# Kernel tuning notes

Hardware: AMD Instinct MI355X
Metric: run time of the kernel (lower is better)

The kernel has to match this reference:

```python
import jax, jax.numpy as jnp
import numpy as np

B, S, D_IN, H, NH, L = 8, 1024, 512, 1024, 16, 4
HD = H // NH
SCALE = HD ** -0.5
EPS = 1e-5


def _ln(x, g, b):
    m = jnp.mean(x, axis=-1, keepdims=True)
    v = jnp.mean((x - m) ** 2, axis=-1, keepdims=True)
    return (x - m) * jax.lax.rsqrt(v + EPS) * g + b


def setup_inputs() -> dict:
    key = jax.random.key(0)
    ks = jax.random.split(key, 12)
    s = lambda k, shape, fan: jax.random.normal(k, shape, jnp.float32) * (fan ** -0.5)
    return {
        "x": jax.random.normal(ks[0], (B, S, D_IN), jnp.float32),
        "W_in": s(ks[1], (D_IN, H), D_IN), "b_in": jnp.zeros((H,), jnp.float32),
        "W_qkv": s(ks[2], (L, H, 3 * H), H), "b_qkv": jnp.zeros((L, 3 * H), jnp.float32),
        "W_o": s(ks[3], (L, H, H), H), "b_o": jnp.zeros((L, H), jnp.float32),
        "g1": jnp.ones((L, H), jnp.float32), "be1": jnp.zeros((L, H), jnp.float32),
        "W_out": s(ks[4], (H, H), H), "b_out": jnp.zeros((H,), jnp.float32),
        "g2": jnp.ones((H,), jnp.float32), "be2": jnp.zeros((H,), jnp.float32),
    }


def _attn_layer(x, Wqkv, bqkv, Wo, bo, g, be):
    b, s, h = x.shape
    qkv = (x @ Wqkv + bqkv).reshape(b, s, 3, NH, HD)
    q = qkv[:, :, 0].transpose(0, 2, 1, 3)  # [B,NH,S,HD]
    k = qkv[:, :, 1].transpose(0, 2, 1, 3)
    v = qkv[:, :, 2].transpose(0, 2, 1, 3)
    scores = jnp.einsum("bhqd,bhkd->bhqk", q, k) * SCALE
    w = jax.nn.softmax(scores, axis=-1)  # dropout is identity in eval
    o = jnp.einsum("bhqk,bhkd->bhqd", w, v)
    o = o.transpose(0, 2, 1, 3).reshape(b, s, h)
    return _ln(o @ Wo + bo + x, g, be)


def reference(x, W_in, b_in, W_qkv, b_qkv, W_o, b_o, g1, be1, W_out, b_out, g2, be2):
    h = x @ W_in + b_in
    for i in range(L):
        h = _attn_layer(h, W_qkv[i], b_qkv[i], W_o[i], b_o[i], g1[i], be1[i])
    pooled = jnp.mean(h, axis=1)  # [B,H]
    return _ln(pooled @ W_out + b_out, g2, be2)
```

## Files before the change

### kernel.cpp

```cpp
#include <hip/hip_runtime.h>
#include <stdint.h>

typedef unsigned short u16;
typedef unsigned int   u32;
typedef __attribute__((ext_vector_type(8))) short short8;
typedef __attribute__((ext_vector_type(4))) float f32x4;
typedef __attribute__((ext_vector_type(16))) float f32x16;
typedef __attribute__((ext_vector_type(2))) unsigned int uint2v;

#define B_   8
#define S_   1024
#define DIN_ 512
#define H_   1024
#define NH_  16
#define HD_  64
#define L_   4
#define M_   (B_*S_)
#define SCALE_ 0.125f
#define EPS_ 1e-5f

__device__ __forceinline__ u16 f2b(float f) {
  u32 u = __builtin_bit_cast(u32, f);
  u32 r = (u + 0x7fffu + ((u >> 16) & 1u)) >> 16;
  return (u16)r;
}

__device__ __forceinline__ u32 cvtpk(float lo, float hi) {
  u32 r;
  asm("v_cvt_pk_bf16_f32 %0, %1, %2" : "=v"(r) : "v"(lo), "v"(hi));
  return r;
}

__device__ __forceinline__ void gll16(const void* g, void* l) {
  __builtin_amdgcn_global_load_lds(
      (const __attribute__((address_space(1))) u32*)(uintptr_t)g,
      (__attribute__((address_space(3))) u32*)(uintptr_t)l,
      16, 0, 0);
}

__global__ void cvt_k(const float* __restrict__ in, u16* __restrict__ out) {
  long i = (long)(blockIdx.x * 256 + threadIdx.x) * 4;
  f32x4 v = *(const f32x4*)&in[i];
  u32 p0 = (u32)f2b(v[0]) | ((u32)f2b(v[1]) << 16);
  u32 p1 = (u32)f2b(v[2]) | ((u32)f2b(v[3]) << 16);
  u32* o = (u32*)&out[i];
  o[0] = p0; o[1] = p1;
}

__global__ __launch_bounds__(256)
void tcvt_k(const float* __restrict__ in0, u16* __restrict__ out0, int R, int C) {
  __shared__ float t[32][33];
  const float* in = in0 + (size_t)blockIdx.z * R * C;
  u16* out = out0 + (size_t)blockIdx.z * R * C;
  int tx = threadIdx.x & 31, ty = threadIdx.x >> 5;
  long r0 = blockIdx.y * 32, c0 = blockIdx.x * 32;
#pragma unroll
  for (int i = 0; i < 4; ++i)
    t[ty + i*8][tx] = in[(r0 + ty + i*8) * (long)C + c0 + tx];
  __syncthreads();
#pragma unroll
  for (int i = 0; i < 4; ++i)
    out[(c0 + ty + i*8) * (long)R + r0 + tx] = f2b(t[tx][ty + i*8]);
}

template<int EPI>
__global__ __launch_bounds__(256, 2)
void gemm_k(const u16* __restrict__ A, const u16* __restrict__ Bt,
            const float* __restrict__ bias,
            float* __restrict__ Cf, u16* __restrict__ Cb,
            const float* __restrict__ Res,
            int Ndim, int K, int scale_cols)
{
  __shared__ u16 As[128 * 32];
  __shared__ u16 Bs[128 * 32];
  const int tid = threadIdx.x;
  const int lane = tid & 63;
  const int wid = tid >> 6;
  const int wr = wid >> 1, wc = wid & 1;
  const int l15 = lane & 15, l4 = lane >> 4;
  const long arow0 = (long)blockIdx.x * 128;
  const long brow0 = (long)blockIdx.y * 128;

  f32x4 acc[4][4] = {};

  const int srow = tid >> 2;
  const int scol = (tid & 3) * 8;
  const u16* ga  = A  + (arow0 + srow) * K + scol;
  const u16* ga1 = ga + 64 * (long)K;
  const u16* gb  = Bt + (brow0 + srow) * K + scol;
  const u16* gb1 = gb + 64 * (long)K;
  u16* lA0 = &As[tid * 8];
  u16* lA1 = &As[2048 + tid * 8];
  u16* lB0 = &Bs[tid * 8];
  u16* lB1 = &Bs[2048 + tid * 8];

  for (int k0 = 0; k0 < K; k0 += 32) {
    gll16(ga + k0, lA0);
    gll16(ga1 + k0, lA1);
    gll16(gb + k0, lB0);
    gll16(gb1 + k0, lB1);
    __syncthreads();
    short8 af[4], bf[4];
#pragma unroll
    for (int m = 0; m < 4; ++m)
      af[m] = *(const short8*)&As[(wr*64 + m*16 + l15) * 32 + l4*8];
#pragma unroll
    for (int n = 0; n < 4; ++n)
      bf[n] = *(const short8*)&Bs[(wc*64 + n*16 + l15) * 32 + l4*8];
#pragma unroll
    for (int m = 0; m < 4; ++m)
#pragma unroll
      for (int n = 0; n < 4; ++n)
        acc[m][n] = __builtin_amdgcn_mfma_f32_16x16x32_bf16(af[m], bf[n], acc[m][n], 0, 0, 0);
    __syncthreads();
  }

  const int crow = wr*64 + l4*4;
  const int ccol = wc*64 + l15;
#pragma unroll
  for (int m = 0; m < 4; ++m) {
#pragma unroll
    for (int n = 0; n < 4; ++n) {
      const int col = (int)brow0 + ccol + n*16;
      const float bv = bias[col];
      const float sc = (EPI == 1 && col < scale_cols) ? SCALE_ : 1.0f;
#pragma unroll
      for (int r = 0; r < 4; ++r) {
        const long row = arow0 + crow + m*16 + r;
        float v = acc[m][n][r] + bv;
        if (EPI == 1) {
          Cb[row * Ndim + col] = f2b(v * sc);
        } else if (EPI == 0) {
          Cf[row * Ndim + col] = v;
          Cb[row * Ndim + col] = f2b(v);
        } else {
          Cf[row * Ndim + col] = v + Res[row * Ndim + col];
        }
      }
    }
  }
}

__global__ __launch_bounds__(512, 1)
void gemm8_k(const u16* __restrict__ A, const u16* __restrict__ Bt,
             const float* __restrict__ bias, u16* __restrict__ Cb)
{
  constexpr int K = 1024, N = 3 * H_;
  constexpr int NT = K / 64;
  __shared__ u16 lds[8][8192];

  const int tid = threadIdx.x;
  const int lane = tid & 63;
  const int wid = tid >> 6;
  const int wm = wid >> 2, wn = wid & 3;
  const int l15 = lane & 15, l4 = lane >> 4;

  const int bid = blockIdx.x;
  const int swz = (bid & 7) * 48 + (bid >> 3);
  const long arow0 = (long)(swz & 31) * 256;
  const long brow0 = (long)(swz >> 5) * 256;

  f32x4 acc[8][4] = {};
  short8 bfr[4][2];
  short8 afr[2][2];

  auto stage = [&](int buf, int op, int half, int kt) {
    const u16* src = op ? Bt : A;
    const long rb = (op ? brow0 : arow0) + half * 128;
    u16* dst = lds[buf*4 + op*2 + half];
#pragma unroll
    for (int ld = 0; ld < 2; ++ld) {
      int p = ld * 512 + tid;
      int row = p >> 3;
      int kc = (p & 7) ^ (row & 7);
      gll16(src + (rb + row) * (long)K + kt * 64 + kc * 8, (char*)dst + p * 16);
    }
  };
  auto readB = [&](int buf) {
    const char* base = (const char*)lds[buf*4 + 2 + (wn >> 1)];
#pragma unroll
    for (int n = 0; n < 4; ++n)
#pragma unroll
      for (int ks = 0; ks < 2; ++ks) {
        int rh = (wn & 1) * 64 + n * 16 + l15;
        int byt = rh * 128 + ((((ks*4 + l4) * 16)) ^ ((rh & 7) << 4));
        bfr[n][ks] = *(const short8*)(base + byt);
      }
  };
  auto readA = [&](int buf, int q) {
    const char* base = (const char*)lds[buf*4 + wm];
#pragma unroll
    for (int j = 0; j < 2; ++j)
#pragma unroll
      for (int ks = 0; ks < 2; ++ks) {
        int rh = (2*q + j) * 16 + l15;
        int byt = rh * 128 + ((((ks*4 + l4) * 16)) ^ ((rh & 7) << 4));
        afr[j][ks] = *(const short8*)(base + byt);
      }
  };
  auto mm = [&](int q) {
    __builtin_amdgcn_s_setprio(1);
#pragma unroll
    for (int j = 0; j < 2; ++j)
#pragma unroll
      for (int n = 0; n < 4; ++n)
#pragma unroll
        for (int ks = 0; ks < 2; ++ks)
          acc[2*q+j][n] = __builtin_amdgcn_mfma_f32_16x16x32_bf16(
              afr[j][ks], bfr[n][ks], acc[2*q+j][n], 0, 0, 0);
    __builtin_amdgcn_s_setprio(0);
  };

#define PH(bufc, q, doB, sb, so, sh, st, doV)                     \
    readA(bufc, q); if (doB) readB(bufc);                         \
    stage(sb, so, sh, st);                                        \
    __builtin_amdgcn_s_barrier();                                 \
    asm volatile("s_waitcnt lgkmcnt(0)" ::: "memory");            \
    __builtin_amdgcn_sched_barrier(0);                            \
    mm(q);                                                        \
    if (doV) asm volatile("s_waitcnt vmcnt(4)" ::: "memory");     \
    __builtin_amdgcn_s_barrier();

  stage(0,0,0,0); stage(0,0,1,0); stage(0,1,0,0); stage(0,1,1,0);
  stage(1,1,0,1); stage(1,1,1,1);
  asm volatile("s_waitcnt vmcnt(4)" ::: "memory");
  __builtin_amdgcn_s_barrier();

  const int niter = NT / 2;
  for (int i = 0; i < niter; ++i) {
    const int t1 = 2*i + 1;
    const int t2 = (2*i + 2 < NT) ? 2*i + 2 : NT - 1;
    const int t3 = (2*i + 3 < NT) ? 2*i + 3 : NT - 1;
    PH(0, 0, true , 1, 0, 0, t1, false)
    PH(0, 1, false, 1, 0, 1, t1, false)
    PH(0, 2, false, 0, 1, 0, t2, false)
    PH(0, 3, false, 0, 1, 1, t2, true )
    PH(1, 0, true , 0, 0, 0, t2, false)
    PH(1, 1, false, 0, 0, 1, t2, false)
    PH(1, 2, false, 1, 1, 0, t3, false)
    PH(1, 3, false, 1, 1, 1, t3, true )
  }
#undef PH

  const long crow0 = arow0 + wm * 128;
  const int  ccol0 = (int)brow0 + wn * 64;
#pragma unroll
  for (int m = 0; m < 8; ++m) {
#pragma unroll
    for (int n = 0; n < 4; ++n) {
      const int col = ccol0 + n * 16 + l15;
      const float bv = bias[col];
      const float sc = (col < H_) ? SCALE_ : 1.0f;
#pragma unroll
      for (int r = 0; r < 4; ++r) {
        const long row = crow0 + m * 16 + l4 * 4 + r;
        Cb[row * N + col] = f2b((acc[m][n][r] + bv) * sc);
      }
    }
  }
}

__global__ __launch_bounds__(512)
void attn_k(const u16* __restrict__ qkv, u16* __restrict__ ob)
{
  __shared__ u16 Ks[2][4096];
  __shared__ u16 Vs[2][4096];

  const int tid = threadIdx.x, lane = tid & 63, wid = tid >> 6;
  const int l31 = lane & 31, hi = lane >> 5;

  const int blk = blockIdx.x;
  const int xcd = blk & 7, slot = blk >> 3;
  const int bh = xcd + ((slot >> 2) << 3);
  const int qx = slot & 3;
  const int b = bh >> 4, nh = bh & 15;
  const int q0 = qx * 256 + wid * 32;

  const int RS = 3 * H_;
  const long base = (long)b * S_ * RS;
  const u16* Qg = qkv + base + nh * HD_;
  const u16* Kg = qkv + base + H_ + nh * HD_;
  const u16* Vg = qkv + base + 2 * H_ + nh * HD_;

  short8 qf[4];
#pragma unroll
  for (int ks = 0; ks < 4; ++ks)
    qf[ks] = *(const short8*)&Qg[(long)(q0 + l31) * RS + ks*16 + hi*8];

  float m_ = -1e30f, l_ = 0.f;
  f32x16 o0 = {}, o1 = {};

  const int krow = tid >> 3, kc = tid & 7;
  const int ksc = kc ^ (krow & 7);
  const long kgoff = (long)krow * RS + ksc * 8;
  const int vd = tid & 63, vch = tid >> 6;
  const int vbyt = (vd*128 + vch*16) ^ ((vd & 7) << 4);

  {
    gll16(Kg + kgoff, (char*)&Ks[0][0] + tid*16);
    union { u16 u[8]; short8 v; } tv;
#pragma unroll
    for (int j = 0; j < 8; ++j)
      tv.u[j] = Vg[(long)(vch*8 + j) * RS + vd];
    *(short8*)((char*)&Vs[0][0] + vbyt) = tv.v;
  }
  __syncthreads();

  for (int t = 0; t < 16; ++t) {
    const int cur = t & 1, nxt = cur ^ 1;
    union { u16 u[8]; short8 v; } ta;
    if (t < 15) {
      const long kv1 = (long)(t + 1) * 64;
      gll16(Kg + kv1 * RS + kgoff, (char*)&Ks[nxt][0] + tid*16);
#pragma unroll
      for (int j = 0; j < 8; ++j)
        ta.u[j] = Vg[(kv1 + vch*8 + j) * RS + vd];
    }

    f32x16 s0 = {}, s1 = {};
    __builtin_amdgcn_s_setprio(1);
#pragma unroll
    for (int ks = 0; ks < 4; ++ks) {
      const int koff = ks*32 + hi*16;
      const int by0 = (l31*128 + koff) ^ ((l31 & 7) << 4);
      short8 kf0 = *(const short8*)((const char*)&Ks[cur][0] + by0);
      s0 = __builtin_amdgcn_mfma_f32_32x32x16_bf16(kf0, qf[ks], s0, 0, 0, 0);
      const int by1 = ((32 + l31)*128 + koff) ^ ((l31 & 7) << 4);
      short8 kf1 = *(const short8*)((const char*)&Ks[cur][0] + by1);
      s1 = __builtin_amdgcn_mfma_f32_32x32x16_bf16(kf1, qf[ks], s1, 0, 0, 0);
    }
    __builtin_amdgcn_s_setprio(0);

    float tmax = -1e30f;
#pragma unroll
    for (int r = 0; r < 16; ++r) tmax = fmaxf(tmax, fmaxf(s0[r], s1[r]));
    tmax = fmaxf(tmax, __shfl_xor(tmax, 32));
    if (!__all(tmax <= m_ + 8.f)) {
      const float mnew = fmaxf(m_, tmax);
      const float corr = __expf(m_ - mnew);
      m_ = mnew; l_ *= corr;
#pragma unroll
      for (int r = 0; r < 16; ++r) {
        float cr = __shfl(corr, (r&3) + 8*(r>>2) + 4*hi);
        o0[r] *= cr; o1[r] *= cr;
      }
    }
    float sum = 0.f;
#pragma unroll
    for (int r = 0; r < 16; ++r) {
      float p0 = __expf(s0[r] - m_);
      float p1 = __expf(s1[r] - m_);
      s0[r] = p0; s1[r] = p1;
      sum += p0 + p1;
    }
    sum += __shfl_xor(sum, 32);
    l_ += sum;

    short8 pa[4];
#pragma unroll
    for (int ks2 = 0; ks2 < 2; ++ks2) {
      const int r0 = 8 * ks2;
      u32 A0 = cvtpk(s0[r0+0], s0[r0+1]), A1 = cvtpk(s0[r0+2], s0[r0+3]);
      u32 B0 = cvtpk(s0[r0+4], s0[r0+5]), B1 = cvtpk(s0[r0+6], s0[r0+7]);
      uint2v w02 = __builtin_amdgcn_permlane32_swap(A0, B0, false, false);
      uint2v w13 = __builtin_amdgcn_permlane32_swap(A1, B1, false, false);
      union { u32 w[4]; short8 v; } u_;
      u_.w[0] = w02.x; u_.w[1] = w13.x; u_.w[2] = w02.y; u_.w[3] = w13.y;
      pa[ks2] = u_.v;
    }
#pragma unroll
    for (int ks2 = 0; ks2 < 2; ++ks2) {
      const int r0 = 8 * ks2;
      u32 A0 = cvtpk(s1[r0+0], s1[r0+1]), A1 = cvtpk(s1[r0+2], s1[r0+3]);
      u32 B0 = cvtpk(s1[r0+4], s1[r0+5]), B1 = cvtpk(s1[r0+6], s1[r0+7]);
      uint2v w02 = __builtin_amdgcn_permlane32_swap(A0, B0, false, false);
      uint2v w13 = __builtin_amdgcn_permlane32_swap(A1, B1, false, false);
      union { u32 w[4]; short8 v; } u_;
      u_.w[0] = w02.x; u_.w[1] = w13.x; u_.w[2] = w02.y; u_.w[3] = w13.y;
      pa[2 + ks2] = u_.v;
    }

    __builtin_amdgcn_s_setprio(1);
#pragma unroll
    for (int ks = 0; ks < 4; ++ks) {
      const int vb = ks*32 + hi*16;
      const int by0 = (l31*128 + vb) ^ ((l31 & 7) << 4);
      short8 v0 = *(const short8*)((const char*)&Vs[cur][0] + by0);
      o0 = __builtin_amdgcn_mfma_f32_32x32x16_bf16(pa[ks], v0, o0, 0, 0, 0);
      const int by1 = ((32 + l31)*128 + vb) ^ ((l31 & 7) << 4);
      short8 v1 = *(const short8*)((const char*)&Vs[cur][0] + by1);
      o1 = __builtin_amdgcn_mfma_f32_32x32x16_bf16(pa[ks], v1, o1, 0, 0, 0);
    }
    __builtin_amdgcn_s_setprio(0);

    if (t < 15) {
      *(short8*)((char*)&Vs[nxt][0] + vbyt) = ta.v;
      __syncthreads();
    }
  }

  const float linv = 1.0f / l_;
#pragma unroll
  for (int r = 0; r < 16; ++r) {
    const int rowq = (r&3) + 8*(r>>2) + 4*hi;
    const float li = __shfl(linv, rowq);
    const long srow = (long)(b * S_ + q0 + rowq);
    ob[srow * H_ + nh*HD_ + l31]      = f2b(o0[r] * li);
    ob[srow * H_ + nh*HD_ + 32 + l31] = f2b(o1[r] * li);
  }
}

__global__ __launch_bounds__(256)
void ln_k(const float* __restrict__ in, const float* __restrict__ g,
          const float* __restrict__ be, float* __restrict__ outf,
          u16* __restrict__ outb, const float* __restrict__ bias)
{
  const int row = blockIdx.x;
  const int tid = threadIdx.x;
  const float* x = in + (long)row * H_;
  f32x4 v = *(const f32x4*)&x[tid * 4];
  if (bias) {
    f32x4 bv = *(const f32x4*)&bias[tid * 4];
    v[0] += bv[0]; v[1] += bv[1]; v[2] += bv[2]; v[3] += bv[3];
  }
  float s  = v[0] + v[1] + v[2] + v[3];
  float ss = v[0]*v[0] + v[1]*v[1] + v[2]*v[2] + v[3]*v[3];
#pragma unroll
  for (int o = 1; o < 64; o <<= 1) {
    s  += __shfl_xor(s, o);
    ss += __shfl_xor(ss, o);
  }
  __shared__ float rs[4], rq[4];
  const int wid = tid >> 6;
  if ((tid & 63) == 0) { rs[wid] = s; rq[wid] = ss; }
  __syncthreads();
  float ts = rs[0] + rs[1] + rs[2] + rs[3];
  float tq = rq[0] + rq[1] + rq[2] + rq[3];
  const float mu = ts * (1.0f / H_);
  const float var = tq * (1.0f / H_) - mu * mu;
  const float rstd = rsqrtf(var + EPS_);
  const long obase = (long)row * H_ + tid * 4;
#pragma unroll
  for (int j = 0; j < 4; ++j) {
    int c = tid * 4 + j;
    float y = (v[j] - mu) * rstd * g[c] + be[c];
    outf[obase + j] = y;
    if (outb) outb[obase + j] = f2b(y);
  }
}

__global__ void pool_k(const float* __restrict__ hf, float* __restrict__ pooled) {
  const int c = blockIdx.x * 256 + threadIdx.x;
  const int b = blockIdx.y;
  const int s0 = blockIdx.z * 128;
  float s = 0.f;
  for (int t = 0; t < 128; ++t) s += hf[((long)(b * S_ + s0 + t)) * H_ + c];
  atomicAdd(&pooled[b * H_ + c], s * (1.0f / S_));
}

__global__ void fgemm_k(const float* __restrict__ pooled, const float* __restrict__ W,
                        float* __restrict__ out) {
  const int n = blockIdx.x * 64 + threadIdx.x;
  const int b = blockIdx.y;
  const int k0 = blockIdx.z * 128;
  const float* pr = pooled + b * H_ + k0;
  const float* wr = W + (long)k0 * H_ + n;
  float s = 0.f;
#pragma unroll 8
  for (int k = 0; k < 128; ++k)
    s += pr[k] * wr[(long)k * H_];
  atomicAdd(&out[b * H_ + n], s);
}

extern "C" void kernel_launch(void* const* d_in, const int* in_sizes, int n_in,
                              void* d_out, int out_size, void* d_ws, size_t ws_size,
                              hipStream_t stream) {
  const float* x     = (const float*)d_in[0];
  const float* W_in  = (const float*)d_in[1];
  const float* b_in  = (const float*)d_in[2];
  const float* W_qkv = (const float*)d_in[3];
  const float* b_qkv = (const float*)d_in[4];
  const float* W_o   = (const float*)d_in[5];
  const float* b_o   = (const float*)d_in[6];
  const float* g1    = (const float*)d_in[7];
  const float* be1   = (const float*)d_in[8];
  const float* W_out = (const float*)d_in[9];
  const float* b_out = (const float*)d_in[10];
  const float* g2    = (const float*)d_in[11];
  const float* be2   = (const float*)d_in[12];
  float* outp = (float*)d_out;

  char* ws = (char*)d_ws;
  float* hf    = (float*)(ws + 0);
  u16*   hb    = (u16*)(ws + 33554432);
  u16*   qkvb  = (u16*)(ws + 50331648);
  float* resf  = (float*)(ws + 50331648);
  u16*   ob    = (u16*)(ws + 100663296);
  u16*   xb    = (u16*)(ws + 100663296);
  u16*   WinT  = (u16*)(ws + 117440512);
  u16*   WqkvT = (u16*)(ws + 118489088);
  u16*   WoT   = (u16*)(ws + 143654912);
  float* pooled= (float*)(ws + 152043520);
  float* tmpf  = (float*)(ws + 152076288);

  cvt_k<<<dim3(M_ * DIN_ / 1024), 256, 0, stream>>>(x, xb);
  tcvt_k<<<dim3(H_/32, DIN_/32, 1), 256, 0, stream>>>(W_in, WinT, DIN_, H_);
  tcvt_k<<<dim3(3*H_/32, H_/32, L_), 256, 0, stream>>>(W_qkv, WqkvT, H_, 3*H_);
  tcvt_k<<<dim3(H_/32, H_/32, L_), 256, 0, stream>>>(W_o, WoT, H_, H_);

  gemm_k<0><<<dim3(M_/128, H_/128), 256, 0, stream>>>(xb, WinT, b_in, hf, hb, nullptr, H_, DIN_, 0);

  for (int l = 0; l < L_; ++l) {
    gemm8_k<<<dim3((M_/256) * (3*H_/256)), 512, 0, stream>>>(hb, WqkvT + (size_t)l*3*H_*H_,
                                                             b_qkv + l*3*H_, qkvb);
    attn_k<<<dim3(512), 512, 0, stream>>>(qkvb, ob);
    gemm_k<2><<<dim3(M_/128, H_/128), 256, 0, stream>>>(ob, WoT + (size_t)l*H_*H_,
                                                        b_o + l*H_, resf, nullptr, hf,
                                                        H_, H_, 0);
    ln_k<<<dim3(M_), 256, 0, stream>>>(resf, g1 + l*H_, be1 + l*H_, hf, hb, nullptr);
  }

  hipMemsetAsync(pooled, 0, B_ * H_ * sizeof(float), stream);
  hipMemsetAsync(tmpf, 0, B_ * H_ * sizeof(float), stream);
  pool_k<<<dim3(H_/256, B_, 8), 256, 0, stream>>>(hf, pooled);
  fgemm_k<<<dim3(H_/64, B_, 8), 64, 0, stream>>>(pooled, W_out, tmpf);
  ln_k<<<dim3(B_), 256, 0, stream>>>(tmpf, g2, be2, outp, nullptr, b_out);
}
```

Before: 876.8 us.

## Deepen QKV GEMM prefetch pipeline, drop lgkmcnt wait, remap blocks per XCD

Changes the block-to-tile mapping so each XCD works on a contiguous group of four A row-tiles, which should improve L2 reuse of A. The global-to-LDS staging schedule is reordered so one more half-tile is in flight, with the vmcnt waits raised from 4 to 6. The explicit lgkmcnt(0) wait and sched_barrier before the MFMA block are removed, leaving LDS-read waits to the compiler. Removing the explicit wait relies on compiler-inserted waits for correctness, and the reordered staging risks LDS buffer hazards if the phase ordering is wrong.

```diff
diff --git a/kernel.cpp b/kernel.cpp
--- a/kernel.cpp
+++ b/kernel.cpp
@@ -156,9 +156,9 @@
   const int l15 = lane & 15, l4 = lane >> 4;
 
   const int bid = blockIdx.x;
-  const int swz = (bid & 7) * 48 + (bid >> 3);
-  const long arow0 = (long)(swz & 31) * 256;
-  const long brow0 = (long)(swz >> 5) * 256;
+  const int xcd = bid & 7, idx = bid >> 3;
+  const long arow0 = (long)(xcd * 4 + (idx & 3)) * 256;
+  const long brow0 = (long)(idx >> 2) * 256;
 
   f32x4 acc[8][4] = {};
   short8 bfr[4][2];
@@ -211,34 +211,32 @@
     __builtin_amdgcn_s_setprio(0);
   };
 
-#define PH(bufc, q, doB, sb, so, sh, st, doV)                     \
-    readA(bufc, q); if (doB) readB(bufc);                         \
+#define PH(cb, q, doB, sb, so, sh, st, doV)                       \
+    readA(cb, q); if (doB) readB(cb);                             \
     stage(sb, so, sh, st);                                        \
     __builtin_amdgcn_s_barrier();                                 \
-    asm volatile("s_waitcnt lgkmcnt(0)" ::: "memory");            \
-    __builtin_amdgcn_sched_barrier(0);                            \
     mm(q);                                                        \
-    if (doV) asm volatile("s_waitcnt vmcnt(4)" ::: "memory");     \
+    if (doV) asm volatile("s_waitcnt vmcnt(6)" ::: "memory");     \
     __builtin_amdgcn_s_barrier();
 
-  stage(0,0,0,0); stage(0,0,1,0); stage(0,1,0,0); stage(0,1,1,0);
-  stage(1,1,0,1); stage(1,1,1,1);
-  asm volatile("s_waitcnt vmcnt(4)" ::: "memory");
+  stage(0,1,0,0); stage(0,1,1,0); stage(0,0,0,0); stage(0,0,1,0);
+  stage(1,1,0,1); stage(1,1,1,1); stage(1,0,0,1);
+  asm volatile("s_waitcnt vmcnt(6)" ::: "memory");
   __builtin_amdgcn_s_barrier();
 
   const int niter = NT / 2;
   for (int i = 0; i < niter; ++i) {
-    const int t1 = 2*i + 1;
-    const int t2 = (2*i + 2 < NT) ? 2*i + 2 : NT - 1;
-    const int t3 = (2*i + 3 < NT) ? 2*i + 3 : NT - 1;
-    PH(0, 0, true , 1, 0, 0, t1, false)
-    PH(0, 1, false, 1, 0, 1, t1, false)
-    PH(0, 2, false, 0, 1, 0, t2, false)
-    PH(0, 3, false, 0, 1, 1, t2, true )
-    PH(1, 0, true , 0, 0, 0, t2, false)
-    PH(1, 1, false, 0, 0, 1, t2, false)
-    PH(1, 2, false, 1, 1, 0, t3, false)
-    PH(1, 3, false, 1, 1, 1, t3, true )
+    const int tO  = 2*i + 1;
+    const int tE2 = (2*i + 2 < NT) ? 2*i + 2 : NT - 1;
+    const int tO2 = (2*i + 3 < NT) ? 2*i + 3 : NT - 1;
+    PH(0, 0, true , 1, 0, 1, tO , false)
+    PH(0, 1, false, 0, 1, 0, tE2, false)
+    PH(0, 2, false, 0, 1, 1, tE2, false)
+    PH(0, 3, false, 0, 0, 0, tE2, true )
+    PH(1, 0, true , 0, 0, 1, tE2, false)
+    PH(1, 1, false, 1, 1, 0, tO2, false)
+    PH(1, 2, false, 1, 1, 1, tO2, false)
+    PH(1, 3, false, 1, 0, 0, tO2, true )
   }
 #undef PH
 
```

Result: no change. 882.0 us (+0.6%).
